# Optimization experiments

Hardware: AMD Instinct MI355X
Metric: run time of the kernel (lower is better)

Reference implementation:

```python
import jax, jax.numpy as jnp
import numpy as np

# Ramamoorthi-Hanrahan irradiance matrix constants
C1d, C2d, C3d, C4d, C5d = 0.429043, 0.511664, 0.743125, 0.886227, 0.247708
# Real SH evaluation constants (degree 0..4), standard plenoxels/3DGS values
_SH_C0 = 0.28209479177387814
_SH_C1 = 0.4886025119029199
_SH_C2 = np.array([1.0925484305920792, -1.0925484305920792, 0.31539156525252005, -1.0925484305920792, 0.5462742152960396], np.float32)
_SH_C3 = np.array([-0.5900435899266435, 2.890611442640554, -0.4570457994644658, 0.3731763325901154, -0.4570457994644658, 1.445305721320277, -0.5900435899266435], np.float32)
_SH_C4 = np.array([2.5033429417967046, -1.7701307697799304, 0.9461746957575601, -0.6690465435572892, 0.10578554691520431, -0.6690465435572892, 0.47308734787878004, -1.7701307697799304, 0.6258357354491761], np.float32)
_L = np.array([l for l in range(5) for _ in range(2 * l + 1)], np.float32)  # SH band index per coeff (25,)
_MI = np.array([0, 0, 0, 0, 1, 1, 1, 2, 2, 3])  # triu_indices(4,4)
_MJ = np.array([0, 1, 2, 3, 1, 2, 3, 2, 3, 3])


def safe_normalize(x, eps=1e-20):
    return x * jax.lax.rsqrt(jnp.maximum(jnp.sum(x * x, -1, keepdims=True), eps))


def sh_basis(d):
    # d: (N,3) directions -> (N,25) real SH basis up to degree 4
    x, y, z = d[..., 0], d[..., 1], d[..., 2]
    xx, yy, zz = x * x, y * y, z * z
    xy, yz, xz = x * y, y * z, x * z
    b = [jnp.full_like(x, _SH_C0),
         -_SH_C1 * y, _SH_C1 * z, -_SH_C1 * x,
         _SH_C2[0] * xy, _SH_C2[1] * yz, _SH_C2[2] * (2.0 * zz - xx - yy), _SH_C2[3] * xz, _SH_C2[4] * (xx - yy),
         _SH_C3[0] * y * (3.0 * xx - yy), _SH_C3[1] * xy * z, _SH_C3[2] * y * (4.0 * zz - xx - yy),
         _SH_C3[3] * z * (2.0 * zz - 3.0 * xx - 3.0 * yy), _SH_C3[4] * x * (4.0 * zz - xx - yy),
         _SH_C3[5] * z * (xx - yy), _SH_C3[6] * x * (xx - 3.0 * yy),
         _SH_C4[0] * xy * (xx - yy), _SH_C4[1] * yz * (3.0 * xx - yy), _SH_C4[2] * xy * (7.0 * zz - 1.0),
         _SH_C4[3] * yz * (7.0 * zz - 3.0), _SH_C4[4] * (zz * (35.0 * zz - 30.0) + 3.0),
         _SH_C4[5] * xz * (7.0 * zz - 3.0), _SH_C4[6] * (xx - yy) * (7.0 * zz - 1.0),
         _SH_C4[7] * xz * (xx - yy), _SH_C4[8] * (xx * (xx - 3.0 * yy) - yy * (3.0 * xx - yy))]
    return jnp.stack(b, -1)


def bilinear_lut(lut, uv):
    # lut: (H,W,2); uv: (N,2) in [0,1]; linear filter, clamp boundary (nvdiffrast texel-center convention)
    H, W, _ = lut.shape
    x = uv[:, 0] * W - 0.5
    y = uv[:, 1] * H - 0.5
    x0 = jnp.floor(x); y0 = jnp.floor(y)
    fx = (x - x0)[:, None]; fy = (y - y0)[:, None]
    x0i = jnp.clip(x0.astype(jnp.int32), 0, W - 1); x1i = jnp.clip(x0i + 1, 0, W - 1)
    y0i = jnp.clip(y0.astype(jnp.int32), 0, H - 1); y1i = jnp.clip(y0i + 1, 0, H - 1)
    v00 = lut[y0i, x0i]; v01 = lut[y0i, x1i]; v10 = lut[y1i, x0i]; v11 = lut[y1i, x1i]
    return (v00 * (1.0 - fx) + v01 * fx) * (1.0 - fy) + (v10 * (1.0 - fx) + v11 * fx) * fy


def shade(gb_pos, gb_normal, albedo, ks, kr, km, view_pos, base, fg_lut):
    wo = safe_normalize(view_pos - gb_pos)
    n = gb_normal
    reflvec = safe_normalize(2.0 * jnp.sum(wo * n, -1, keepdims=True) * n - wo)
    # --- diffuse irradiance: n_h^T M n_h per color channel (RH quadratic form) ---
    n_h = jnp.concatenate([n, jnp.ones_like(n[:, :1])], -1)  # (N,4)
    e = base  # (25,3)
    triu = jnp.stack([C1d * e[8], C1d * e[4], C1d * e[7], C2d * e[3], -C1d * e[8],
                      C1d * e[5], C2d * e[1], C3d * e[6], C2d * e[2], C4d * e[0] - C5d * e[6]], 0)  # (10,3)
    M = jnp.zeros((4, 4, 3), base.dtype).at[_MI, _MJ].set(triu).at[_MJ, _MI].set(triu)  # symmetric (4,4,3)
    diffuse_irr = jnp.einsum('ni,ijc,nj->nc', n_h, M, n_h)  # (N,3)
    diffuse = albedo * diffuse_irr
    # --- specular ---
    NdotV = jnp.maximum(jnp.sum(wo * n, -1, keepdims=True), 1e-4)
    fg = bilinear_lut(fg_lut, jnp.concatenate([NdotV, kr], -1))  # (N,2)
    gwk = jnp.exp(-(_L * (_L + 1.0))[None, :] * (kr * kr))  # (N,25) Gauss-Weierstrass kernel per SH band
    spec_irr = gwk[:, :, None] * base[None]  # (N,25,3)
    spec_rad = jnp.einsum('nk,nkc->nc', sh_basis(reflvec), spec_irr)  # (N,3)
    F0 = (1.0 - km) * 0.04 + albedo * km
    reflectance = F0 * fg[:, :1] + fg[:, 1:2]
    spec = spec_rad * reflectance
    rgb = jax.nn.sigmoid(diffuse + spec)
    return rgb, diffuse, spec


def setup_inputs() -> dict:
    key = jax.random.key(0)
    k = jax.random.split(key, 9)
    N = 1048576  # 1024x1024 pixels
    return {
        'gb_pos': jax.random.normal(k[0], (N, 3), jnp.float32),
        'gb_normal': jax.random.normal(k[1], (N, 3), jnp.float32),
        'albedo': jax.random.uniform(k[2], (N, 3), jnp.float32),
        'ks': jax.random.uniform(k[3], (N, 1), jnp.float32),
        'kr': jax.random.uniform(k[4], (N, 1), jnp.float32),
        'km': jax.random.uniform(k[5], (N, 1), jnp.float32),
        'view_pos': jax.random.normal(k[6], (N, 3), jnp.float32),
        'base': jax.random.normal(k[7], (25, 3), jnp.float32) * 0.5,
        'fg_lut': jax.random.uniform(k[8], (256, 256, 2), jnp.float32),
    }


def reference(gb_pos, gb_normal, albedo, ks, kr, km, view_pos, base, fg_lut):
    return shade(gb_pos, gb_normal, albedo, ks, kr, km, view_pos, base, fg_lut)
```

## Files before the change

kernel.cpp:

```cpp
#include <hip/hip_runtime.h>
#include <math.h>


__device__ __forceinline__ void shade_pixel(
    float px, float py, float pz,
    float nx, float ny, float nz,
    float ax, float ay, float az,
    float krv, float kmv,
    float vx, float vy, float vz,
    const float* __restrict__ eb, const float* __restrict__ fg_lut,
    float* rgb, float* dif, float* spc)
{
    float wx = vx - px, wy = vy - py, wz = vz - pz;
    float wl2 = wx*wx + wy*wy + wz*wz;
    float winv = __builtin_amdgcn_rsqf(fmaxf(wl2, 1e-20f));
    wx *= winv; wy *= winv; wz *= winv;

    float ndv = wx*nx + wy*ny + wz*nz;

    float rx = 2.0f*ndv*nx - wx;
    float ry = 2.0f*ndv*ny - wy;
    float rz = 2.0f*ndv*nz - wz;
    float rl2 = rx*rx + ry*ry + rz*rz;
    float rinv = __builtin_amdgcn_rsqf(fmaxf(rl2, 1e-20f));
    rx *= rinv; ry *= rinv; rz *= rinv;

    float NdotV = fmaxf(ndv, 1e-4f);
    float xf = NdotV * 256.0f - 0.5f;
    float yf = krv   * 256.0f - 0.5f;
    float x0f = floorf(xf), y0f = floorf(yf);
    float fx = xf - x0f, fy = yf - y0f;
    int x0i = min(max((int)x0f, 0), 255);
    int x1i = min(x0i + 1, 255);
    int y0i = min(max((int)y0f, 0), 255);
    int y1i = min(y0i + 1, 255);
    const float2* lut2 = (const float2*)fg_lut;
    float2 t00 = lut2[(y0i << 8) + x0i];
    float2 t01 = lut2[(y0i << 8) + x1i];
    float2 t10 = lut2[(y1i << 8) + x0i];
    float2 t11 = lut2[(y1i << 8) + x1i];
    float gxw = 1.0f - fx, gyw = 1.0f - fy;
    float fg0 = (t00.x*gxw + t01.x*fx)*gyw + (t10.x*gxw + t11.x*fx)*fy;
    float fg1 = (t00.y*gxw + t01.y*fx)*gyw + (t10.y*gxw + t11.y*fx)*fy;

    float k2 = krv*krv;
    float g1 = __expf( -2.0f*k2);
    float g2 = __expf( -6.0f*k2);
    float g3 = __expf(-12.0f*k2);
    float g4 = __expf(-20.0f*k2);

    float xx = rx*rx, yy = ry*ry, zz = rz*rz;
    float xy = rx*ry, yz = ry*rz, xz = rx*rz;

    float sr0 = 0.0f, sr1 = 0.0f, sr2 = 0.0f;
#define SHACC(K, EXPR) do { float bk_ = (EXPR);                      \
        sr0 = fmaf(bk_, eb[3*(K)+0], sr0);                           \
        sr1 = fmaf(bk_, eb[3*(K)+1], sr1);                           \
        sr2 = fmaf(bk_, eb[3*(K)+2], sr2); } while (0)

    SHACC(0,  0.28209479177387814f);
    SHACC(1,  (-0.4886025119029199f*ry) * g1);
    SHACC(2,  ( 0.4886025119029199f*rz) * g1);
    SHACC(3,  (-0.4886025119029199f*rx) * g1);
    SHACC(4,  ( 1.0925484305920792f*xy) * g2);
    SHACC(5,  (-1.0925484305920792f*yz) * g2);
    SHACC(6,  ( 0.31539156525252005f*(2.0f*zz - xx - yy)) * g2);
    SHACC(7,  (-1.0925484305920792f*xz) * g2);
    SHACC(8,  ( 0.5462742152960396f*(xx - yy)) * g2);
    SHACC(9,  (-0.5900435899266435f*ry*(3.0f*xx - yy)) * g3);
    SHACC(10, ( 2.890611442640554f*xy*rz) * g3);
    SHACC(11, (-0.4570457994644658f*ry*(4.0f*zz - xx - yy)) * g3);
    SHACC(12, ( 0.3731763325901154f*rz*(2.0f*zz - 3.0f*xx - 3.0f*yy)) * g3);
    SHACC(13, (-0.4570457994644658f*rx*(4.0f*zz - xx - yy)) * g3);
    SHACC(14, ( 1.445305721320277f*rz*(xx - yy)) * g3);
    SHACC(15, (-0.5900435899266435f*rx*(xx - 3.0f*yy)) * g3);
    SHACC(16, ( 2.5033429417967046f*xy*(xx - yy)) * g4);
    SHACC(17, (-1.7701307697799304f*yz*(3.0f*xx - yy)) * g4);
    SHACC(18, ( 0.9461746957575601f*xy*(7.0f*zz - 1.0f)) * g4);
    SHACC(19, (-0.6690465435572892f*yz*(7.0f*zz - 3.0f)) * g4);
    SHACC(20, ( 0.10578554691520431f*(zz*(35.0f*zz - 30.0f) + 3.0f)) * g4);
    SHACC(21, (-0.6690465435572892f*xz*(7.0f*zz - 3.0f)) * g4);
    SHACC(22, ( 0.47308734787878004f*(xx - yy)*(7.0f*zz - 1.0f)) * g4);
    SHACC(23, (-1.7701307697799304f*xz*(xx - yy)) * g4);
    SHACC(24, ( 0.6258357354491761f*(xx*(xx - 3.0f*yy) - yy*(3.0f*xx - yy))) * g4);
#undef SHACC

    float q0  = nx*nx - ny*ny;
    float qz  = nz*nz;
    float qxy = nx*ny, qxz = nx*nz, qyz = ny*nz;

    float alb[3] = {ax, ay, az};
    float srs[3] = {sr0, sr1, sr2};
    #pragma unroll
    for (int c = 0; c < 3; ++c) {
        float e0 = eb[0*3+c], e1 = eb[1*3+c], e2 = eb[2*3+c], e3 = eb[3*3+c],
              e4 = eb[4*3+c], e5 = eb[5*3+c], e6 = eb[6*3+c], e7 = eb[7*3+c],
              e8 = eb[8*3+c];
        float irr = 0.429043f*e8*q0 + 0.743125f*e6*qz + (0.886227f*e0 - 0.247708f*e6)
                  + 2.0f*(0.429043f*(e4*qxy + e7*qxz + e5*qyz)
                        + 0.511664f*(e3*nx + e1*ny + e2*nz));
        float dc = alb[c] * irr;

        float F0 = (1.0f - kmv)*0.04f + alb[c]*kmv;
        float sc = srs[c] * (F0*fg0 + fg1);

        float v = dc + sc;
        rgb[c] = __builtin_amdgcn_rcpf(1.0f + __expf(-v));
        dif[c] = dc;
        spc[c] = sc;
    }
}

__global__ __launch_bounds__(256) void shade_kernel(
    const float* __restrict__ gb_pos, const float* __restrict__ gb_normal,
    const float* __restrict__ albedo, const float* __restrict__ kr,
    const float* __restrict__ km, const float* __restrict__ view_pos,
    const float* __restrict__ base, const float* __restrict__ fg_lut,
    float* __restrict__ out, int N)
{
    __shared__ float s_pos[768], s_nrm[768], s_alb[768], s_view[768];
    __shared__ float s_kr[256], s_km[256];

    const int t   = threadIdx.x;
    const int blk = blockIdx.x;
    const int p0  = blk << 8;

    float* out_rgb = out;
    float* out_dif = out + (size_t)3 * N;
    float* out_spc = out + (size_t)6 * N;

    if (p0 + 256 <= N) {
        if (t < 192) {
            const size_t b4 = (size_t)blk * 192 + t;
            ((float4*)s_pos )[t] = ((const float4*)gb_pos   )[b4];
            ((float4*)s_nrm )[t] = ((const float4*)gb_normal)[b4];
            ((float4*)s_alb )[t] = ((const float4*)albedo   )[b4];
            ((float4*)s_view)[t] = ((const float4*)view_pos )[b4];
        } else {
            const int u = t - 192;
            const size_t k4 = (size_t)blk * 64 + u;
            ((float4*)s_kr)[u] = ((const float4*)kr)[k4];
            ((float4*)s_km)[u] = ((const float4*)km)[k4];
        }
        __syncthreads();

        float px = s_pos[3*t],  py = s_pos[3*t+1],  pz = s_pos[3*t+2];
        float nx = s_nrm[3*t],  ny = s_nrm[3*t+1],  nz = s_nrm[3*t+2];
        float ax = s_alb[3*t],  ay = s_alb[3*t+1],  az = s_alb[3*t+2];
        float vx = s_view[3*t], vy = s_view[3*t+1], vz = s_view[3*t+2];
        float krv = s_kr[t], kmv = s_km[t];
        __syncthreads();

        float R[3], D[3], S[3];
        shade_pixel(px, py, pz, nx, ny, nz, ax, ay, az, krv, kmv,
                    vx, vy, vz, base, fg_lut, R, D, S);

        s_pos[3*t] = R[0]; s_pos[3*t+1] = R[1]; s_pos[3*t+2] = R[2];
        s_nrm[3*t] = D[0]; s_nrm[3*t+1] = D[1]; s_nrm[3*t+2] = D[2];
        s_alb[3*t] = S[0]; s_alb[3*t+1] = S[1]; s_alb[3*t+2] = S[2];
        __syncthreads();

        if (t < 192) {
            const size_t b4 = (size_t)blk * 192 + t;
            ((float4*)out_rgb)[b4] = ((float4*)s_pos)[t];
            ((float4*)out_dif)[b4] = ((float4*)s_nrm)[t];
            ((float4*)out_spc)[b4] = ((float4*)s_alb)[t];
        }
    } else {
        const int p = p0 + t;
        if (p < N) {
            float R[3], D[3], S[3];
            shade_pixel(gb_pos[3*p], gb_pos[3*p+1], gb_pos[3*p+2],
                        gb_normal[3*p], gb_normal[3*p+1], gb_normal[3*p+2],
                        albedo[3*p], albedo[3*p+1], albedo[3*p+2],
                        kr[p], km[p],
                        view_pos[3*p], view_pos[3*p+1], view_pos[3*p+2],
                        base, fg_lut, R, D, S);
            for (int c = 0; c < 3; ++c) {
                out_rgb[3*p+c] = R[c];
                out_dif[3*p+c] = D[c];
                out_spc[3*p+c] = S[c];
            }
        }
    }
}

extern "C" void kernel_launch(void* const* d_in, const int* in_sizes, int n_in,
                              void* d_out, int out_size, void* d_ws, size_t ws_size,
                              hipStream_t stream) {
    const float* gb_pos    = (const float*)d_in[0];
    const float* gb_normal = (const float*)d_in[1];
    const float* albedo    = (const float*)d_in[2];
    const float* kr        = (const float*)d_in[4];
    const float* km        = (const float*)d_in[5];
    const float* view_pos  = (const float*)d_in[6];
    const float* base      = (const float*)d_in[7];
    const float* fg_lut    = (const float*)d_in[8];
    float* out = (float*)d_out;

    int N = in_sizes[0] / 3;
    int block = 256;
    int grid = (N + block - 1) / block;
    shade_kernel<<<grid, block, 0, stream>>>(gb_pos, gb_normal, albedo, kr, km,
                                             view_pos, base, fg_lut, out, N);
}
```

Before: 123.2 us.

## Use nontemporal vector loads/stores and separate output LDS buffers to drop a barrier

Global input loads and output stores now use nontemporal builtins on 4-wide vectors, hinting the cache to skip retaining streaming data. Results are written to dedicated shared-memory output arrays, so the second __syncthreads between reading inputs and writing results is removed. The LUT bilinear blend is moved after the SH accumulation to give the gather loads more time to land. The extra 9 KB of LDS per block may reduce occupancy.

```diff
diff --git a/kernel.cpp b/kernel.cpp
--- a/kernel.cpp
+++ b/kernel.cpp
@@ -1,6 +1,8 @@
 #include <hip/hip_runtime.h>
 #include <math.h>
 
+
+typedef float f4_t __attribute__((ext_vector_type(4)));
 
 __device__ __forceinline__ void shade_pixel(
     float px, float py, float pz,
@@ -39,9 +41,6 @@
     float2 t01 = lut2[(y0i << 8) + x1i];
     float2 t10 = lut2[(y1i << 8) + x0i];
     float2 t11 = lut2[(y1i << 8) + x1i];
-    float gxw = 1.0f - fx, gyw = 1.0f - fy;
-    float fg0 = (t00.x*gxw + t01.x*fx)*gyw + (t10.x*gxw + t11.x*fx)*fy;
-    float fg1 = (t00.y*gxw + t01.y*fx)*gyw + (t10.y*gxw + t11.y*fx)*fy;
 
     float k2 = krv*krv;
     float g1 = __expf( -2.0f*k2);
@@ -85,6 +84,10 @@
     SHACC(24, ( 0.6258357354491761f*(xx*(xx - 3.0f*yy) - yy*(3.0f*xx - yy))) * g4);
 #undef SHACC
 
+    float gxw = 1.0f - fx, gyw = 1.0f - fy;
+    float fg0 = (t00.x*gxw + t01.x*fx)*gyw + (t10.x*gxw + t11.x*fx)*fy;
+    float fg1 = (t00.y*gxw + t01.y*fx)*gyw + (t10.y*gxw + t11.y*fx)*fy;
+
     float q0  = nx*nx - ny*ny;
     float qz  = nz*nz;
     float qxy = nx*ny, qxz = nx*nz, qyz = ny*nz;
@@ -120,6 +123,7 @@
 {
     __shared__ float s_pos[768], s_nrm[768], s_alb[768], s_view[768];
     __shared__ float s_kr[256], s_km[256];
+    __shared__ float s_rgb[768], s_dif[768], s_spc[768];
 
     const int t   = threadIdx.x;
     const int blk = blockIdx.x;
@@ -132,39 +136,36 @@
     if (p0 + 256 <= N) {
         if (t < 192) {
             const size_t b4 = (size_t)blk * 192 + t;
-            ((float4*)s_pos )[t] = ((const float4*)gb_pos   )[b4];
-            ((float4*)s_nrm )[t] = ((const float4*)gb_normal)[b4];
-            ((float4*)s_alb )[t] = ((const float4*)albedo   )[b4];
-            ((float4*)s_view)[t] = ((const float4*)view_pos )[b4];
+            ((f4_t*)s_pos )[t] = __builtin_nontemporal_load((const f4_t*)gb_pos    + b4);
+            ((f4_t*)s_nrm )[t] = __builtin_nontemporal_load((const f4_t*)gb_normal + b4);
+            ((f4_t*)s_alb )[t] = __builtin_nontemporal_load((const f4_t*)albedo    + b4);
+            ((f4_t*)s_view)[t] = __builtin_nontemporal_load((const f4_t*)view_pos  + b4);
         } else {
             const int u = t - 192;
             const size_t k4 = (size_t)blk * 64 + u;
-            ((float4*)s_kr)[u] = ((const float4*)kr)[k4];
-            ((float4*)s_km)[u] = ((const float4*)km)[k4];
+            ((f4_t*)s_kr)[u] = __builtin_nontemporal_load((const f4_t*)kr + k4);
+            ((f4_t*)s_km)[u] = __builtin_nontemporal_load((const f4_t*)km + k4);
         }
         __syncthreads();
 
-        float px = s_pos[3*t],  py = s_pos[3*t+1],  pz = s_pos[3*t+2];
-        float nx = s_nrm[3*t],  ny = s_nrm[3*t+1],  nz = s_nrm[3*t+2];
-        float ax = s_alb[3*t],  ay = s_alb[3*t+1],  az = s_alb[3*t+2];
-        float vx = s_view[3*t], vy = s_view[3*t+1], vz = s_view[3*t+2];
-        float krv = s_kr[t], kmv = s_km[t];
-        __syncthreads();
-
         float R[3], D[3], S[3];
-        shade_pixel(px, py, pz, nx, ny, nz, ax, ay, az, krv, kmv,
-                    vx, vy, vz, base, fg_lut, R, D, S);
-
-        s_pos[3*t] = R[0]; s_pos[3*t+1] = R[1]; s_pos[3*t+2] = R[2];
-        s_nrm[3*t] = D[0]; s_nrm[3*t+1] = D[1]; s_nrm[3*t+2] = D[2];
-        s_alb[3*t] = S[0]; s_alb[3*t+1] = S[1]; s_alb[3*t+2] = S[2];
+        shade_pixel(s_pos[3*t],  s_pos[3*t+1],  s_pos[3*t+2],
+                    s_nrm[3*t],  s_nrm[3*t+1],  s_nrm[3*t+2],
+                    s_alb[3*t],  s_alb[3*t+1],  s_alb[3*t+2],
+                    s_kr[t],     s_km[t],
+                    s_view[3*t], s_view[3*t+1], s_view[3*t+2],
+                    base, fg_lut, R, D, S);
+
+        s_rgb[3*t] = R[0]; s_rgb[3*t+1] = R[1]; s_rgb[3*t+2] = R[2];
+        s_dif[3*t] = D[0]; s_dif[3*t+1] = D[1]; s_dif[3*t+2] = D[2];
+        s_spc[3*t] = S[0]; s_spc[3*t+1] = S[1]; s_spc[3*t+2] = S[2];
         __syncthreads();
 
         if (t < 192) {
             const size_t b4 = (size_t)blk * 192 + t;
-            ((float4*)out_rgb)[b4] = ((float4*)s_pos)[t];
-            ((float4*)out_dif)[b4] = ((float4*)s_nrm)[t];
-            ((float4*)out_spc)[b4] = ((float4*)s_alb)[t];
+            __builtin_nontemporal_store(((f4_t*)s_rgb)[t], (f4_t*)out_rgb + b4);
+            __builtin_nontemporal_store(((f4_t*)s_dif)[t], (f4_t*)out_dif + b4);
+            __builtin_nontemporal_store(((f4_t*)s_spc)[t], (f4_t*)out_spc + b4);
         }
     } else {
         const int p = p0 + t;
```

Result: slower. 125.8 us (+2.1%).
